# Optimization experiments

Measured on AMD Instinct MI355X. Metric: run time of the kernel, lower is better.

## Reference

```python
import jax, jax.numpy as jnp
import numpy as np


def setup_inputs() -> dict:
    key = jax.random.key(0)
    k1, k2 = jax.random.split(key)
    B, N, M, D = 16, 2048, 2048, 3
    predictions = jax.random.normal(k1, (B, N, D), dtype=jnp.float32)
    targets = jax.random.normal(k2, (B, M, D), dtype=jnp.float32)
    return {"predictions": predictions, "targets": targets}


def reference(predictions, targets):
    # Batched pairwise squared distances: [B, N, M]
    # d(i,j) = |x_i|^2 + |y_j|^2 - 2 x_i . y_j
    xx = jnp.sum(predictions * predictions, axis=-1)  # [B, N]
    yy = jnp.sum(targets * targets, axis=-1)          # [B, M]
    xy = jnp.einsum("bnd,bmd->bnm", predictions, targets)  # [B, N, M]
    P = xx[:, :, None] + yy[:, None, :] - 2.0 * xy    # [B, N, M]
    # Chamfer: sum of per-point nearest-neighbor squared distances, both directions
    loss = jnp.sum(jnp.min(P, axis=2)) + jnp.sum(jnp.min(P, axis=1))
    return loss
```

## Files before the change

kernel.cpp:

```cpp
#include <hip/hip_runtime.h>
#include <math.h>


typedef float v2f __attribute__((ext_vector_type(2)));

#define NPTS    2048
#define NCOMBO  32
#define KSLICE  16
#define SLICE   128
#define SPT     8

__device__ __forceinline__ v2f pkfma(v2f a, v2f b, v2f c) {
#if __has_builtin(__builtin_elementwise_fma)
    return __builtin_elementwise_fma(a, b, c);
#else
    v2f d; d.x = fmaf(a.x, b.x, c.x); d.y = fmaf(a.y, b.y, c.y); return d;
#endif
}

__global__ __launch_bounds__(256, 2) void chamfer_partial(
    const float* __restrict__ preds,
    const float* __restrict__ tgts,
    float* __restrict__ partial,
    float* __restrict__ out)
{
    __shared__ __align__(16) float qx[SLICE];
    __shared__ __align__(16) float qy[SLICE];
    __shared__ __align__(16) float qz[SLICE];
    __shared__ __align__(16) float qw[SLICE];

    const int bid   = blockIdx.x;
    const int combo = bid & (NCOMBO - 1);
    const int slice = bid >> 5;
    const int dir   = combo >> 4;
    const int b     = combo & 15;

    if (bid == 0 && threadIdx.x == 0) out[0] = 0.0f;

    const float* src = (dir ? tgts : preds) + (size_t)b * NPTS * 3;
    const float* opp = (dir ? preds : tgts) + (size_t)b * NPTS * 3;

    if (threadIdx.x < SLICE) {
        const int jj = slice * SLICE + threadIdx.x;
        const float y0 = opp[3 * jj + 0];
        const float y1 = opp[3 * jj + 1];
        const float y2 = opp[3 * jj + 2];
        qx[threadIdx.x] = y0;
        qy[threadIdx.x] = y1;
        qz[threadIdx.x] = y2;
        qw[threadIdx.x] = y0 * y0 + y1 * y1 + y2 * y2;
    }

    v2f nn0[SPT], nn1[SPT], nn2[SPT];
    float m[SPT];
    #pragma unroll
    for (int k = 0; k < SPT; k++) {
        const int i = threadIdx.x + 256 * k;
        const float a0 = -2.0f * src[3 * i + 0];
        const float a1 = -2.0f * src[3 * i + 1];
        const float a2 = -2.0f * src[3 * i + 2];
        nn0[k] = (v2f){a0, a0};
        nn1[k] = (v2f){a1, a1};
        nn2[k] = (v2f){a2, a2};
        m[k]   = INFINITY;
    }
    __syncthreads();

    #pragma unroll 2
    for (int jg = 0; jg < SLICE / 4; jg++) {
        const float4 X = *(const float4*)&qx[4 * jg];
        const float4 Y = *(const float4*)&qy[4 * jg];
        const float4 Z = *(const float4*)&qz[4 * jg];
        const float4 W = *(const float4*)&qw[4 * jg];
        const v2f Xa = {X.x, X.y}, Xb = {X.z, X.w};
        const v2f Ya = {Y.x, Y.y}, Yb = {Y.z, Y.w};
        const v2f Za = {Z.x, Z.y}, Zb = {Z.z, Z.w};
        const v2f Wa = {W.x, W.y}, Wb = {W.z, W.w};
        #pragma unroll
        for (int k = 0; k < SPT; k++) {
            const v2f sa = pkfma(nn0[k], Xa, pkfma(nn1[k], Ya, pkfma(nn2[k], Za, Wa)));
            m[k] = fminf(fminf(m[k], sa.x), sa.y);
            const v2f sb = pkfma(nn0[k], Xb, pkfma(nn1[k], Yb, pkfma(nn2[k], Zb, Wb)));
            m[k] = fminf(fminf(m[k], sb.x), sb.y);
        }
    }

    float* pp = partial + ((size_t)combo * KSLICE + slice) * NPTS;
    #pragma unroll
    for (int k = 0; k < SPT; k++)
        pp[threadIdx.x + 256 * k] = m[k];
}

__global__ __launch_bounds__(256) void chamfer_reduce(
    const float* __restrict__ preds,
    const float* __restrict__ tgts,
    const float* __restrict__ partial,
    float* __restrict__ out)
{
    __shared__ float wsum[4];

    const int idx   = blockIdx.x * 256 + threadIdx.x;
    const int combo = idx >> 11;
    const int i     = idx & (NPTS - 1);
    const int dir   = combo >> 4;
    const int b     = combo & 15;

    const float* src = (dir ? tgts : preds) + (size_t)b * NPTS * 3;
    const float x0 = src[3 * i + 0];
    const float x1 = src[3 * i + 1];
    const float x2 = src[3 * i + 2];
    const float xx = x0 * x0 + x1 * x1 + x2 * x2;

    const float* pp = partial + (size_t)combo * KSLICE * NPTS + i;
    float mn = pp[0];
    #pragma unroll
    for (int s = 1; s < KSLICE; s++)
        mn = fminf(mn, pp[(size_t)s * NPTS]);

    float val = xx + mn;

    #pragma unroll
    for (int off = 32; off > 0; off >>= 1)
        val += __shfl_down(val, off, 64);

    const int lane = threadIdx.x & 63;
    const int wid  = threadIdx.x >> 6;
    if (lane == 0) wsum[wid] = val;
    __syncthreads();
    if (threadIdx.x == 0)
        atomicAdd(out, wsum[0] + wsum[1] + wsum[2] + wsum[3]);
}

extern "C" void kernel_launch(void* const* d_in, const int* in_sizes, int n_in,
                              void* d_out, int out_size, void* d_ws, size_t ws_size,
                              hipStream_t stream) {
    const float* preds = (const float*)d_in[0];
    const float* tgts  = (const float*)d_in[1];
    float* out     = (float*)d_out;
    float* partial = (float*)d_ws;

    chamfer_partial<<<NCOMBO * KSLICE, 256, 0, stream>>>(preds, tgts, partial, out);
    chamfer_reduce<<<(2 * 16 * NPTS) / 256, 256, 0, stream>>>(preds, tgts, partial, out);
}
```

Baseline: 70.75 us.

## Fuse partial-min and reduce kernels with full opposite set in shared memory

Each block now loads the entire opposite point set (2048 points) into padded shared memory and handles 64 source points. Threads split the opposite set across 32 groups, and the per-source minimum is reduced with shuffles and shared memory inside the block. This removes the global partial buffer and the second reduce kernel, and the output is zeroed with a memset. In exchange, every block reloads the full opposite set and uses about 35KB of shared memory, so fewer blocks can be resident per CU.

```diff
diff --git a/kernel.cpp b/kernel.cpp
--- a/kernel.cpp
+++ b/kernel.cpp
@@ -4,11 +4,13 @@
 
 typedef float v2f __attribute__((ext_vector_type(2)));
 
-#define NPTS    2048
-#define NCOMBO  32
-#define KSLICE  16
-#define SLICE   128
-#define SPT     8
+#define NPTS   2048
+#define NCOMBO 32
+#define SRCB   64
+#define SPT    8
+#define NQ     32
+#define OPPT   (NPTS/NQ)
+#define PAD(i) ((i) + (((i) >> 6) << 2))
 
 __device__ __forceinline__ v2f pkfma(v2f a, v2f b, v2f c) {
 #if __has_builtin(__builtin_elementwise_fma)
@@ -18,47 +20,49 @@
 #endif
 }
 
-__global__ __launch_bounds__(256, 2) void chamfer_partial(
+__global__ __launch_bounds__(256, 4) void chamfer_fused(
     const float* __restrict__ preds,
     const float* __restrict__ tgts,
-    float* __restrict__ partial,
     float* __restrict__ out)
 {
-    __shared__ __align__(16) float qx[SLICE];
-    __shared__ __align__(16) float qy[SLICE];
-    __shared__ __align__(16) float qz[SLICE];
-    __shared__ __align__(16) float qw[SLICE];
+    __shared__ __align__(16) float qx[2176];
+    __shared__ __align__(16) float qy[2176];
+    __shared__ __align__(16) float qz[2176];
+    __shared__ __align__(16) float qw[2176];
+    __shared__ float sm[4 * SRCB];
 
-    const int bid   = blockIdx.x;
-    const int combo = bid & (NCOMBO - 1);
-    const int slice = bid >> 5;
+    const int combo = blockIdx.x & (NCOMBO - 1);
+    const int chunk = blockIdx.x >> 5;
     const int dir   = combo >> 4;
     const int b     = combo & 15;
-
-    if (bid == 0 && threadIdx.x == 0) out[0] = 0.0f;
 
     const float* src = (dir ? tgts : preds) + (size_t)b * NPTS * 3;
     const float* opp = (dir ? preds : tgts) + (size_t)b * NPTS * 3;
 
-    if (threadIdx.x < SLICE) {
-        const int jj = slice * SLICE + threadIdx.x;
-        const float y0 = opp[3 * jj + 0];
-        const float y1 = opp[3 * jj + 1];
-        const float y2 = opp[3 * jj + 2];
-        qx[threadIdx.x] = y0;
-        qy[threadIdx.x] = y1;
-        qz[threadIdx.x] = y2;
-        qw[threadIdx.x] = y0 * y0 + y1 * y1 + y2 * y2;
+    #pragma unroll
+    for (int p = 0; p < NPTS / 256; p++) {
+        const int i = threadIdx.x + 256 * p;
+        const float y0 = opp[3 * i + 0];
+        const float y1 = opp[3 * i + 1];
+        const float y2 = opp[3 * i + 2];
+        const int pi = PAD(i);
+        qx[pi] = y0;
+        qy[pi] = y1;
+        qz[pi] = y2;
+        qw[pi] = y0 * y0 + y1 * y1 + y2 * y2;
     }
+
+    const int q = threadIdx.x >> 3;
+    const int c = threadIdx.x & 7;
 
     v2f nn0[SPT], nn1[SPT], nn2[SPT];
     float m[SPT];
     #pragma unroll
     for (int k = 0; k < SPT; k++) {
-        const int i = threadIdx.x + 256 * k;
-        const float a0 = -2.0f * src[3 * i + 0];
-        const float a1 = -2.0f * src[3 * i + 1];
-        const float a2 = -2.0f * src[3 * i + 2];
+        const int s = chunk * SRCB + c * SPT + k;
+        const float a0 = -2.0f * src[3 * s + 0];
+        const float a1 = -2.0f * src[3 * s + 1];
+        const float a2 = -2.0f * src[3 * s + 2];
         nn0[k] = (v2f){a0, a0};
         nn1[k] = (v2f){a1, a1};
         nn2[k] = (v2f){a2, a2};
@@ -66,12 +70,13 @@
     }
     __syncthreads();
 
+    const int base = q * 68;
     #pragma unroll 2
-    for (int jg = 0; jg < SLICE / 4; jg++) {
-        const float4 X = *(const float4*)&qx[4 * jg];
-        const float4 Y = *(const float4*)&qy[4 * jg];
-        const float4 Z = *(const float4*)&qz[4 * jg];
-        const float4 W = *(const float4*)&qw[4 * jg];
+    for (int g = 0; g < OPPT / 4; g++) {
+        const float4 X = *(const float4*)&qx[base + 4 * g];
+        const float4 Y = *(const float4*)&qy[base + 4 * g];
+        const float4 Z = *(const float4*)&qz[base + 4 * g];
+        const float4 W = *(const float4*)&qw[base + 4 * g];
         const v2f Xa = {X.x, X.y}, Xb = {X.z, X.w};
         const v2f Ya = {Y.x, Y.y}, Yb = {Y.z, Y.w};
         const v2f Za = {Z.x, Z.y}, Zb = {Z.z, Z.w};
@@ -85,50 +90,37 @@
         }
     }
 
-    float* pp = partial + ((size_t)combo * KSLICE + slice) * NPTS;
     #pragma unroll
-    for (int k = 0; k < SPT; k++)
-        pp[threadIdx.x + 256 * k] = m[k];
-}
-
-__global__ __launch_bounds__(256) void chamfer_reduce(
-    const float* __restrict__ preds,
-    const float* __restrict__ tgts,
-    const float* __restrict__ partial,
-    float* __restrict__ out)
-{
-    __shared__ float wsum[4];
-
-    const int idx   = blockIdx.x * 256 + threadIdx.x;
-    const int combo = idx >> 11;
-    const int i     = idx & (NPTS - 1);
-    const int dir   = combo >> 4;
-    const int b     = combo & 15;
-
-    const float* src = (dir ? tgts : preds) + (size_t)b * NPTS * 3;
-    const float x0 = src[3 * i + 0];
-    const float x1 = src[3 * i + 1];
-    const float x2 = src[3 * i + 2];
-    const float xx = x0 * x0 + x1 * x1 + x2 * x2;
-
-    const float* pp = partial + (size_t)combo * KSLICE * NPTS + i;
-    float mn = pp[0];
-    #pragma unroll
-    for (int s = 1; s < KSLICE; s++)
-        mn = fminf(mn, pp[(size_t)s * NPTS]);
-
-    float val = xx + mn;
-
-    #pragma unroll
-    for (int off = 32; off > 0; off >>= 1)
-        val += __shfl_down(val, off, 64);
-
+    for (int k = 0; k < SPT; k++) {
+        float v = m[k];
+        v = fminf(v, __shfl_xor(v, 8, 64));
+        v = fminf(v, __shfl_xor(v, 16, 64));
+        v = fminf(v, __shfl_xor(v, 32, 64));
+        m[k] = v;
+    }
     const int lane = threadIdx.x & 63;
     const int wid  = threadIdx.x >> 6;
-    if (lane == 0) wsum[wid] = val;
+    if (lane < 8) {
+        #pragma unroll
+        for (int k = 0; k < SPT; k++)
+            sm[wid * SRCB + c * SPT + k] = m[k];
+    }
     __syncthreads();
-    if (threadIdx.x == 0)
-        atomicAdd(out, wsum[0] + wsum[1] + wsum[2] + wsum[3]);
+
+    if (threadIdx.x < 64) {
+        const int off = (threadIdx.x & 7) * SPT + (threadIdx.x >> 3);
+        float mn = fminf(fminf(sm[off],            sm[SRCB + off]),
+                         fminf(sm[2 * SRCB + off], sm[3 * SRCB + off]));
+        const int s = chunk * SRCB + off;
+        const float x0 = src[3 * s + 0];
+        const float x1 = src[3 * s + 1];
+        const float x2 = src[3 * s + 2];
+        float val = x0 * x0 + x1 * x1 + x2 * x2 + mn;
+        #pragma unroll
+        for (int o = 32; o > 0; o >>= 1)
+            val += __shfl_down(val, o, 64);
+        if (threadIdx.x == 0) atomicAdd(out, val);
+    }
 }
 
 extern "C" void kernel_launch(void* const* d_in, const int* in_sizes, int n_in,
@@ -136,9 +128,8 @@
                               hipStream_t stream) {
     const float* preds = (const float*)d_in[0];
     const float* tgts  = (const float*)d_in[1];
-    float* out     = (float*)d_out;
-    float* partial = (float*)d_ws;
+    float* out = (float*)d_out;
 
-    chamfer_partial<<<NCOMBO * KSLICE, 256, 0, stream>>>(preds, tgts, partial, out);
-    chamfer_reduce<<<(2 * 16 * NPTS) / 256, 256, 0, stream>>>(preds, tgts, partial, out);
+    hipMemsetAsync(out, 0, sizeof(float), stream);
+    chamfer_fused<<<NCOMBO * 32, 256, 0, stream>>>(preds, tgts, out);
 }
```

After: 75.01 us. 6.0% more time.
